# Kernel optimization log

Hardware: AMD Instinct MI355X
Metric: run time of the kernel (lower is better)

Reference implementation:

```python
import jax, jax.numpy as jnp
import numpy as np

D = 256; H = 4; HD = 64; WBAND = 64; KLOC = 8; EMAK = 256
SUMDECAY = 0.9; STATEDECAY = 0.9; STEP = 0.5


def _dwconv(x, kern, pad):
    # x: (B,T,D), kern: (D,1,K) cross-correlation taps, causal left pad
    lhs = jnp.transpose(x, (0, 2, 1))
    out = jax.lax.conv_general_dilated(
        lhs, kern, (1,), [(pad, 0)],
        dimension_numbers=('NCH', 'OIH', 'NCH'),
        feature_group_count=x.shape[-1])
    return jnp.transpose(out, (0, 2, 1))


def _ln(x, g, b):
    m = jnp.mean(x, -1, keepdims=True)
    v = jnp.var(x, -1, keepdims=True)
    return (x - m) * jax.lax.rsqrt(v + 1e-5) * g + b


def _lin(x, w, b):
    return jnp.dot(x, w.T) + b


def _forward(parallel_repr, sequential_state, trajectory_summary, conv_w, conv_b,
             qkv_w, qkv_b, mo_w, mo_b, fg_w, fg_b, gkv_w, gkv_b, go_w, go_b,
             comb_w, comb_b, ffn1_w, ffn1_b, ffn2_w, ffn2_b, tr1_w, tr1_b,
             tr2_w, tr2_b, p2s_w, p2s_b, s2p_w, s2p_b,
             ln1_g, ln1_b, ln2_g, ln2_b, ln3_g, ln3_b, ln4_g, ln4_b):
    B, T, _ = parallel_repr.shape
    # Tier 1: local depthwise causal conv (window 8); torch pads both sides then slices [:T] == causal left pad
    local_history = _dwconv(parallel_repr, conv_w, KLOC - 1) + conv_b
    # Tier 2: banded causal attention (keep j in [i-63, i])
    qkv = _lin(parallel_repr, qkv_w, qkv_b).reshape(B, T, 3, H, HD)
    qkv = jnp.transpose(qkv, (2, 0, 3, 1, 4))  # (3,B,H,T,HD)
    q, k, v = qkv[0], qkv[1], qkv[2]
    idx = jnp.arange(T)
    band = (idx[:, None] >= idx[None, :]) & (idx[None, :] > idx[:, None] - WBAND)
    scores = jnp.einsum('bhqd,bhkd->bhqk', q, k) / jnp.sqrt(jnp.float32(HD))
    attn = jax.nn.softmax(jnp.where(band, scores, -1e9), -1)
    med = jnp.einsum('bhqk,bhkd->bhqd', attn, v)
    med = jnp.transpose(med, (0, 2, 1, 3)).reshape(B, T, D)
    med = _lin(med, mo_w, mo_b)
    fg = jax.nn.sigmoid(_lin(jnp.concatenate([parallel_repr, med], -1), fg_w, fg_b))
    medium_out = med * fg
    # Tier 3: causal cumulative (linear-attention style) global concepts
    gkv = _lin(parallel_repr, gkv_w, gkv_b)
    gk, gv = jnp.split(gkv, 2, -1)
    gk = jax.nn.elu(gk) + 1.0
    concepts = jnp.cumsum(gk * gv, 1) / (jnp.cumsum(gk, 1) + 1e-5)
    global_out = _lin(concepts, go_w, go_b)
    combined = _lin(jnp.concatenate([local_history, medium_out, global_out], -1), comb_w, comb_b)
    pr = _ln(parallel_repr + combined, ln1_g, ln1_b)
    # EMA summary via 256-tap causal depthwise conv: w[i] = (1-d)*d^i
    kE = min(T, EMAK)
    taps = (1.0 - SUMDECAY) * SUMDECAY ** jnp.arange(kE, dtype=jnp.float32)
    kern = jnp.broadcast_to(taps[::-1][None, None, :], (D, 1, kE))
    global_summary = _dwconv(pr, kern, kE - 1)
    guidance = _lin(pr, p2s_w, p2s_b)
    cs = jnp.concatenate([pr + 0.3 * guidance, global_summary], -1)
    deltas = jnp.tanh(_lin(jax.nn.gelu(_lin(cs, tr1_w, tr1_b), approximate=False), tr2_w, tr2_b))
    scaled = deltas * STEP
    # state accumulation via conv trick: acc[t] = sum_i d^i * delta[t-i]
    staps = STATEDECAY ** jnp.arange(kE, dtype=jnp.float32)
    skern = jnp.broadcast_to(staps[::-1][None, None, :], (D, 1, kE))
    acc = _dwconv(scaled, skern, kE - 1)
    dpow = STATEDECAY ** jnp.arange(1, T + 1, dtype=jnp.float32)
    pre_ln = sequential_state[:, None, :] * dpow[None, :, None] + acc
    states = _ln(pre_ln, ln3_g, ln3_b)
    seq_g = _lin(states, s2p_w, s2p_b)
    ffn = _lin(jax.nn.gelu(_lin(pr + 0.3 * seq_g, ffn1_w, ffn1_b), approximate=False), ffn2_w, ffn2_b)
    pr_out = _ln(pr + ffn, ln2_g, ln2_b)
    final_state = _ln(states[:, -1, :], ln4_g, ln4_b)
    final_traj = global_summary[:, -1, :]
    return pr_out, final_state, final_traj


def setup_inputs():
    key = jax.random.key(0)
    ks = jax.random.split(key, 20)
    B, T = 4, 2048
    s = 0.02
    def w(i, shape):
        return jax.random.normal(ks[i], shape, jnp.float32) * s
    return {
        'parallel_repr': jax.random.normal(ks[0], (B, T, D), jnp.float32),
        'sequential_state': jax.random.normal(ks[1], (B, D), jnp.float32),
        'trajectory_summary': jax.random.normal(ks[2], (B, D), jnp.float32),
        'conv_w': w(3, (D, 1, KLOC)), 'conv_b': jnp.zeros((D,)),
        'qkv_w': w(4, (3 * D, D)), 'qkv_b': jnp.zeros((3 * D,)),
        'mo_w': w(5, (D, D)), 'mo_b': jnp.zeros((D,)),
        'fg_w': w(6, (D, 2 * D)), 'fg_b': jnp.zeros((D,)),
        'gkv_w': w(7, (2 * D, D)), 'gkv_b': jnp.zeros((2 * D,)),
        'go_w': w(8, (D, D)), 'go_b': jnp.zeros((D,)),
        'comb_w': w(9, (D, 3 * D)), 'comb_b': jnp.zeros((D,)),
        'ffn1_w': w(10, (4 * D, D)), 'ffn1_b': jnp.zeros((4 * D,)),
        'ffn2_w': w(11, (D, 4 * D)), 'ffn2_b': jnp.zeros((D,)),
        'tr1_w': w(12, (2 * D, 2 * D)), 'tr1_b': jnp.zeros((2 * D,)),
        'tr2_w': w(13, (D, 2 * D)), 'tr2_b': jnp.zeros((D,)),
        'p2s_w': w(14, (D, D)), 'p2s_b': jnp.zeros((D,)),
        's2p_w': w(15, (D, D)), 's2p_b': jnp.zeros((D,)),
        'ln1_g': jnp.ones((D,)), 'ln1_b': jnp.zeros((D,)),
        'ln2_g': jnp.ones((D,)), 'ln2_b': jnp.zeros((D,)),
        'ln3_g': jnp.ones((D,)), 'ln3_b': jnp.zeros((D,)),
        'ln4_g': jnp.ones((D,)), 'ln4_b': jnp.zeros((D,)),
    }


def reference(parallel_repr, sequential_state, trajectory_summary, conv_w, conv_b,
              qkv_w, qkv_b, mo_w, mo_b, fg_w, fg_b, gkv_w, gkv_b, go_w, go_b,
              comb_w, comb_b, ffn1_w, ffn1_b, ffn2_w, ffn2_b, tr1_w, tr1_b,
              tr2_w, tr2_b, p2s_w, p2s_b, s2p_w, s2p_b,
              ln1_g, ln1_b, ln2_g, ln2_b, ln3_g, ln3_b, ln4_g, ln4_b):
    return _forward(parallel_repr, sequential_state, trajectory_summary, conv_w, conv_b,
                    qkv_w, qkv_b, mo_w, mo_b, fg_w, fg_b, gkv_w, gkv_b, go_w, go_b,
                    comb_w, comb_b, ffn1_w, ffn1_b, ffn2_w, ffn2_b, tr1_w, tr1_b,
                    tr2_w, tr2_b, p2s_w, p2s_b, s2p_w, s2p_b,
                    ln1_g, ln1_b, ln2_g, ln2_b, ln3_g, ln3_b, ln4_g, ln4_b)
```

## Files before the change

kernel.cpp:

```cpp
#include <hip/hip_runtime.h>
#include <hip/hip_bf16.h>
#include <math.h>

#define D_  256
#define T_  2048
#define B_  4
#define M_  (B_*T_)
#define H_  4
#define HD_ 64

#define NC_ 64
#define LCH (T_/NC_)

enum { OP_NONE=0, OP_SIGMUL=1, OP_ADDAUX=2, OP_AXPBY=3, OP_GELU=4, OP_TANHHALF=5 };

typedef unsigned short u16;
typedef short short8 __attribute__((ext_vector_type(8)));
typedef float f32x4  __attribute__((ext_vector_type(4)));

__device__ __forceinline__ float gelu_f(float x){ return 0.5f*x*(1.0f+erff(x*0.70710678118654752f)); }
__device__ __forceinline__ float sigmoid_f(float x){ return 1.0f/(1.0f+expf(-x)); }

__device__ __forceinline__ unsigned pk2(float a, float b){
    __hip_bfloat162 h = __float22bfloat162_rn(make_float2(a,b));
    union { __hip_bfloat162 h; unsigned u; } c; c.h = h; return c.u;
}
__device__ __forceinline__ float bfu(u16 u){ return __uint_as_float(((unsigned)u)<<16); }
__device__ __forceinline__ u16 bf1(float x){ return (u16)(pk2(x,x)&0xffffu); }

#define OFF_QKV   0u
#define OFF_MO    327680u
#define OFF_FG    393216u
#define OFF_GO    524288u
#define OFF_COMB  589824u
#define OFF_FFN1  786432u
#define OFF_FFN2  1048576u
#define OFF_TR1   1310720u
#define OFF_TR2   1572864u
#define OFF_P2S   1703936u
#define OFF_S2P   1769472u
#define NWELEM    1835008u
#define NXELEM    2097152u

__global__ __launch_bounds__(256) void cvt_k(
    const float* __restrict__ qkv_w, const float* __restrict__ gkv_w,
    const float* __restrict__ qkv_b, const float* __restrict__ gkv_b,
    const float* __restrict__ mo_w,  const float* __restrict__ fg_w,
    const float* __restrict__ go_w,  const float* __restrict__ comb_w,
    const float* __restrict__ ffn1_w,const float* __restrict__ ffn2_w,
    const float* __restrict__ tr1_w, const float* __restrict__ tr2_w,
    const float* __restrict__ p2s_w, const float* __restrict__ s2p_w,
    const float* __restrict__ X,
    u16* __restrict__ Wh, u16* __restrict__ Xh, float* __restrict__ bq)
{
    size_t i = ((size_t)blockIdx.x*256 + threadIdx.x)*4;
    if (i < NWELEM){
        const float* s; size_t base;
        if      (i < OFF_MO)  { s=(i<196608)?qkv_w:gkv_w; base=(i<196608)?0:196608; }
        else if (i < OFF_FG)  { s=mo_w;   base=OFF_MO; }
        else if (i < OFF_GO)  { s=fg_w;   base=OFF_FG; }
        else if (i < OFF_COMB){ s=go_w;   base=OFF_GO; }
        else if (i < OFF_FFN1){ s=comb_w; base=OFF_COMB; }
        else if (i < OFF_FFN2){ s=ffn1_w; base=OFF_FFN1; }
        else if (i < OFF_TR1) { s=ffn2_w; base=OFF_FFN2; }
        else if (i < OFF_TR2) { s=tr1_w;  base=OFF_TR1; }
        else if (i < OFF_P2S) { s=tr2_w;  base=OFF_TR2; }
        else if (i < OFF_S2P) { s=p2s_w;  base=OFF_P2S; }
        else                  { s=s2p_w;  base=OFF_S2P; }
        float4 v = *(const float4*)(s + (i-base));
        *(uint2*)(Wh + i) = (uint2){ pk2(v.x,v.y), pk2(v.z,v.w) };
    } else if (i < NWELEM + NXELEM){
        size_t j = i - NWELEM;
        float4 v = *(const float4*)(X + j);
        *(uint2*)(Xh + j) = (uint2){ pk2(v.x,v.y), pk2(v.z,v.w) };
    } else if (i < NWELEM + NXELEM + 1280){
        size_t j = i - (NWELEM + NXELEM);
        #pragma unroll
        for (int k=0;k<4;++k){
            size_t e = j + k;
            bq[e] = (e < 768) ? qkv_b[e] : gkv_b[e-768];
        }
    }
}

__global__ __launch_bounds__(256) void gemm_k(
    const u16* __restrict__ A0, const u16* __restrict__ W0, int ldw0, int K0,
    const u16* __restrict__ A1, const u16* __restrict__ W1, int ldw1, int K1,
    const u16* __restrict__ A2, const u16* __restrict__ W2, int ldw2, int K2,
    const float* __restrict__ bias, const void* __restrict__ aux, int aux_bf16,
    void* __restrict__ C, int ldc, int c_bf16, int op, int ncol, u16* __restrict__ vt)
{
    __shared__ u16 As[64*64];
    __shared__ u16 Ws[64*64];

    const int q8   = gridDim.x >> 3;
    const int lid  = (blockIdx.x & 7)*q8 + (blockIdx.x >> 3);
    const int brow = lid / ncol;
    const int bcol = lid - brow*ncol;
    const int row0 = brow*64, col0 = bcol*64;

    const int tid  = threadIdx.x;
    const int lane = tid & 63, wid = tid >> 6;
    const int wm = (wid >> 1)*32, wn = (wid & 1)*32;
    const int l15 = lane & 15, l4 = lane >> 4;
    const int srow = tid >> 3;
    const int sc8  = (tid & 7) * 8;

    f32x4 acc[2][2];
    #pragma unroll
    for (int i=0;i<2;++i)
        #pragma unroll
        for (int j=0;j<2;++j) acc[i][j] = (f32x4){0.f,0.f,0.f,0.f};

    uint4 ra0, ra1, rw0, rw1;

    auto loadtile = [&](const u16* A, const u16* W, int ldw, int K, int kb){
        const u16* ga = A + (size_t)(row0+srow)*K + kb + sc8;
        ra0 = *(const uint4*)ga;
        ra1 = *(const uint4*)(ga + (size_t)32*K);
        const u16* gw = W + (size_t)(col0+srow)*ldw + kb + sc8;
        rw0 = *(const uint4*)gw;
        rw1 = *(const uint4*)(gw + (size_t)32*ldw);
    };
    auto storetile = [&](){
        const int i0 = (srow*64 + sc8) ^ ((srow&7)<<3);
        *(uint4*)&As[i0] = ra0;  *(uint4*)&Ws[i0] = rw0;
        const int r2 = srow + 32;
        const int i1 = (r2*64 + sc8) ^ ((r2&7)<<3);
        *(uint4*)&As[i1] = ra1;  *(uint4*)&Ws[i1] = rw1;
    };
    auto mfma_tile = [&](){
        #pragma unroll
        for (int ks=0;ks<2;++ks){
            const int koff = ks*32 + l4*8;
            short8 af[2], bf[2];
            #pragma unroll
            for (int f=0;f<2;++f){
                const int ar = wm + f*16 + l15;
                af[f] = *(const short8*)&As[(ar*64 + koff) ^ ((ar&7)<<3)];
                const int brn = wn + f*16 + l15;
                bf[f] = *(const short8*)&Ws[(brn*64 + koff) ^ ((brn&7)<<3)];
            }
            #pragma unroll
            for (int fm=0;fm<2;++fm)
                #pragma unroll
                for (int fn=0;fn<2;++fn)
                    acc[fm][fn] = __builtin_amdgcn_mfma_f32_16x16x32_bf16(
                        af[fm], bf[fn], acc[fm][fn], 0, 0, 0);
        }
    };

    const u16* Ac = A0; const u16* Wc = W0; int ldwc = ldw0, Kc = K0, kb = 0;
    loadtile(Ac, Wc, ldwc, Kc, 0);
    while (true){
        __syncthreads();
        storetile();
        __syncthreads();
        int nkb = kb + 64;
        const u16* nA = Ac; const u16* nW = Wc; int nld = ldwc, nK = Kc;
        bool have_next = true;
        if (nkb >= Kc){
            if (Ac == A0 && A1){ nA = A1; nW = W1; nld = ldw1; nK = K1; nkb = 0; }
            else if (Ac == A1 && A2){ nA = A2; nW = W2; nld = ldw2; nK = K2; nkb = 0; }
            else have_next = false;
        }
        if (have_next) loadtile(nA, nW, nld, nK, nkb);
        mfma_tile();
        if (!have_next) break;
        Ac = nA; Wc = nW; ldwc = nld; Kc = nK; kb = nkb;
    }

    #pragma unroll
    for (int fn=0;fn<2;++fn){
        const int n = col0 + wn + fn*16 + l15;
        const float bv = bias[n];
        const bool vwr = (vt != nullptr) && (n >= 512) && (n < 768);
        #pragma unroll
        for (int fm=0;fm<2;++fm){
            #pragma unroll
            for (int j=0;j<4;++j){
                const int m = row0 + wm + fm*16 + l4*4 + j;
                float v = acc[fm][fn][j] + bv;
                if (op==OP_GELU)          v = gelu_f(v);
                else if (op==OP_TANHHALF) v = 0.5f*tanhf(v);
                else if (op!=OP_NONE){
                    const size_t ai = (size_t)m*D_ + n;
                    const float a = aux_bf16 ? bfu(((const u16*)aux)[ai])
                                             : ((const float*)aux)[ai];
                    if (op==OP_SIGMUL)      v = a*sigmoid_f(v);
                    else if (op==OP_ADDAUX) v = v + a;
                    else                    v = a + 0.3f*v;
                }
                if (c_bf16) ((u16*)C)[(size_t)m*ldc + n] = bf1(v);
                else        ((float*)C)[(size_t)m*ldc + n] = v;
                if (vwr){
                    const int hh = (n-512)>>6, dd = (n-512)&63;
                    const int bb = m >> 11, tt = m & (T_-1);
                    vt[(((size_t)(bb*H_ + hh))*64 + dd)*T_ + tt] = bf1(v);
                }
            }
        }
    }
}

__global__ __launch_bounds__(256) void conv_k(const float* __restrict__ X,
    const float* __restrict__ w, const float* __restrict__ bias, u16* __restrict__ out)
{
    int idx = blockIdx.x*256 + threadIdx.x;
    int d = idx & (D_-1);
    int bt = idx >> 8;
    int t = bt & (T_-1);
    float acc = bias[d];
    const float* xp = X + (size_t)bt*D_ + d;
    const float* wp = w + d*8;
    #pragma unroll
    for (int j=0;j<8;++j){
        int tt = t - 7 + j;
        if (tt >= 0) acc += xp[(size_t)(j-7)*D_] * wp[j];
    }
    out[idx] = bf1(acc);
}

__global__ __launch_bounds__(256) void attn_k(const u16* __restrict__ QKVG,
    const u16* __restrict__ VT, u16* __restrict__ MED)
{
    __shared__ u16 Kl[128*64];
    __shared__ u16 Ql[64*64];
    __shared__ u16 Vl[64*128];
    const int b = blockIdx.z, h = blockIdx.y;
    const int t0 = blockIdx.x * 64;
    const int kb0 = t0 - 64;
    const int tid = threadIdx.x;

    {
        const int r0 = tid >> 3, c8 = (tid & 7) * 8;
        #pragma unroll
        for (int rep=0;rep<4;++rep){
            const int r = r0 + rep*32;
            const int kg = kb0 + r;
            uint4 pk = {0,0,0,0};
            if (kg >= 0)
                pk = *(const uint4*)(QKVG + ((size_t)(b*T_ + kg))*1280 + 256 + h*HD_ + c8);
            *(uint4*)&Kl[(r*64 + c8) ^ ((r&7)<<3)] = pk;
        }
        #pragma unroll
        for (int rep=0;rep<2;++rep){
            const int r = r0 + rep*32;
            uint4 pq = *(const uint4*)(QKVG + ((size_t)(b*T_ + t0 + r))*1280 + h*HD_ + c8);
            *(uint4*)&Ql[(r*64 + c8) ^ ((r&7)<<3)] = pq;
        }
    }
    {
        const int d0 = tid >> 4, c8 = (tid & 15) * 8;
        #pragma unroll
        for (int rep=0;rep<4;++rep){
            const int d = d0 + rep*16;
            uint4 pv = {0,0,0,0};
            if (kb0 + c8 >= 0)
                pv = *(const uint4*)(VT + ((size_t)((b*H_ + h)*64 + d))*T_ + kb0 + c8);
            *(uint4*)&Vl[(d*128 + c8) ^ ((d&7)<<3)] = pv;
        }
    }
    __syncthreads();

    const int lane = tid & 63, w = tid >> 6;
    const int l15 = lane & 15, l4 = lane >> 4;

    short8 bq[2];
    {
        const int qr = w*16 + l15;
        bq[0] = *(const short8*)&Ql[(qr*64 +      l4*8) ^ ((qr&7)<<3)];
        bq[1] = *(const short8*)&Ql[(qr*64 + 32 + l4*8) ^ ((qr&7)<<3)];
    }

    f32x4 s[8];
    #pragma unroll
    for (int kf=0;kf<8;++kf){
        const int kr = kf*16 + l15;
        short8 a0 = *(const short8*)&Kl[(kr*64 +      l4*8) ^ ((kr&7)<<3)];
        short8 a1 = *(const short8*)&Kl[(kr*64 + 32 + l4*8) ^ ((kr&7)<<3)];
        f32x4 acc = (f32x4){0.f,0.f,0.f,0.f};
        acc = __builtin_amdgcn_mfma_f32_16x16x32_bf16(a0, bq[0], acc, 0,0,0);
        acc = __builtin_amdgcn_mfma_f32_16x16x32_bf16(a1, bq[1], acc, 0,0,0);
        s[kf] = acc;
    }

    const int qg = t0 + w*16 + l15;
    float m = -1e30f;
    #pragma unroll
    for (int kf=0;kf<8;++kf){
        #pragma unroll
        for (int j=0;j<4;++j){
            const int kg = kb0 + kf*16 + l4*4 + j;
            const int diff = qg - kg;
            const float v = (kg >= 0 && diff >= 0 && diff < 64) ? s[kf][j]*0.125f : -1e30f;
            s[kf][j] = v;
            m = fmaxf(m, v);
        }
    }
    m = fmaxf(m, __shfl_xor(m,16));
    m = fmaxf(m, __shfl_xor(m,32));
    float lsum = 0.f;
    unsigned lo[8], hi[8];
    #pragma unroll
    for (int kf=0;kf<8;++kf){
        const float p0 = expf(s[kf][0]-m), p1 = expf(s[kf][1]-m);
        const float p2 = expf(s[kf][2]-m), p3 = expf(s[kf][3]-m);
        lsum += (p0+p1)+(p2+p3);
        lo[kf] = pk2(p0,p1);
        hi[kf] = pk2(p2,p3);
    }
    lsum += __shfl_xor(lsum,16);
    lsum += __shfl_xor(lsum,32);
    const float inv = 1.f/lsum;

    f32x4 o[4];
    #pragma unroll
    for (int df=0;df<4;++df) o[df] = (f32x4){0.f,0.f,0.f,0.f};
    const int baseLane = l15 + ((l4&1)<<5);
    const bool hiHalf = (l4>>1) != 0;
    #pragma unroll
    for (int kb=0;kb<4;++kb){
        const int x0 = __shfl((int)lo[2*kb],   baseLane);
        const int x1 = __shfl((int)hi[2*kb],   baseLane);
        const int x2 = __shfl((int)lo[2*kb],   baseLane+16);
        const int x3 = __shfl((int)hi[2*kb],   baseLane+16);
        const int y0 = __shfl((int)lo[2*kb+1], baseLane);
        const int y1 = __shfl((int)hi[2*kb+1], baseLane);
        const int y2 = __shfl((int)lo[2*kb+1], baseLane+16);
        const int y3 = __shfl((int)hi[2*kb+1], baseLane+16);
        int4 afi;
        afi.x = hiHalf ? y0 : x0;
        afi.y = hiHalf ? y1 : x1;
        afi.z = hiHalf ? y2 : x2;
        afi.w = hiHalf ? y3 : x3;
        union { int4 i; short8 s; } cv; cv.i = afi;
        #pragma unroll
        for (int df=0;df<4;++df){
            const int vr = df*16 + l15;
            short8 bv = *(const short8*)&Vl[(vr*128 + kb*32 + l4*8) ^ ((vr&7)<<3)];
            o[df] = __builtin_amdgcn_mfma_f32_16x16x32_bf16(cv.s, bv, o[df], 0,0,0);
        }
    }

    #pragma unroll
    for (int j=0;j<4;++j){
        const float invj = __shfl(inv, l4*4 + j);
        const int mrow = b*T_ + t0 + w*16 + l4*4 + j;
        u16* op = MED + (size_t)mrow*D_ + h*HD_ + l15;
        #pragma unroll
        for (int df=0;df<4;++df)
            op[df*16] = bf1(o[df][j] * invj);
    }
}

__global__ __launch_bounds__(256) void scan1_p1(const u16* __restrict__ QKVG,
    float* __restrict__ CA, float* __restrict__ CC)
{
    const int d = threadIdx.x, c = blockIdx.x, b = blockIdx.y;
    const u16* base = QKVG + ((size_t)(b*T_ + c*LCH))*1280;
    float sgk=0.f, sgkv=0.f;
    for (int t=0;t<LCH;++t){
        float gk = bfu(base[(size_t)t*1280 + 768 + d]);
        gk = gk > 0.f ? gk + 1.f : expf(gk);
        float gv = bfu(base[(size_t)t*1280 + 1024 + d]);
        sgk += gk; sgkv += gk*gv;
    }
    CA[((size_t)b*NC_ + c)*D_ + d] = sgk;
    CC[((size_t)b*NC_ + c)*D_ + d] = sgkv;
}

__global__ void scan1_p2(float* __restrict__ CA, float* __restrict__ CC)
{
    int idx = blockIdx.x*256 + threadIdx.x;
    int d = idx & (D_-1), b = idx >> 8;
    float sa=0.f, sc=0.f;
    for (int c=0;c<NC_;++c){
        size_t o = ((size_t)b*NC_ + c)*D_ + d;
        float a = CA[o], cc = CC[o];
        CA[o] = sa; CC[o] = sc;
        sa += a; sc += cc;
    }
}

__global__ __launch_bounds__(256) void scan1_p3(const u16* __restrict__ QKVG,
    const float* __restrict__ CA, const float* __restrict__ CC, u16* __restrict__ CONC)
{
    const int d = threadIdx.x, c = blockIdx.x, b = blockIdx.y;
    float sgk  = CA[((size_t)b*NC_ + c)*D_ + d];
    float sgkv = CC[((size_t)b*NC_ + c)*D_ + d];
    const u16* base = QKVG + ((size_t)(b*T_ + c*LCH))*1280;
    u16* out = CONC + ((size_t)(b*T_ + c*LCH))*D_ + d;
    for (int t=0;t<LCH;++t){
        float gk = bfu(base[(size_t)t*1280 + 768 + d]);
        gk = gk > 0.f ? gk + 1.f : expf(gk);
        float gv = bfu(base[(size_t)t*1280 + 1024 + d]);
        sgk += gk; sgkv += gk*gv;
        out[(size_t)t*D_] = bf1(sgkv / (sgk + 1e-5f));
    }
}

__global__ __launch_bounds__(256) void ema_p1(const float* __restrict__ X,
    float* __restrict__ CARRY, float alpha)
{
    const int d = threadIdx.x, c = blockIdx.x, b = blockIdx.y;
    const float* xp = X + ((size_t)(b*T_ + c*LCH))*D_ + d;
    float g = 0.f;
    for (int t=0;t<LCH;++t) g = 0.9f*g + alpha*xp[(size_t)t*D_];
    CARRY[((size_t)b*NC_ + c)*D_ + d] = g;
}

__global__ void ema_p2(float* __restrict__ CARRY, float* __restrict__ traj)
{
    int idx = blockIdx.x*256 + threadIdx.x;
    int d = idx & (D_-1), b = idx >> 8;
    const float dL = powf(0.9f, (float)LCH);
    float run = 0.f;
    for (int c=0;c<NC_;++c){
        size_t o = ((size_t)b*NC_ + c)*D_ + d;
        float loc = CARRY[o];
        CARRY[o] = run;
        run = loc + dL*run;
    }
    if (traj) traj[b*D_ + d] = run;
}

__global__ __launch_bounds__(256) void ema_p3h(const float* __restrict__ X,
    const float* __restrict__ CARRY, u16* __restrict__ OUT, float alpha)
{
    const int d = threadIdx.x, c = blockIdx.x, b = blockIdx.y;
    float g = CARRY[((size_t)b*NC_ + c)*D_ + d];
    const float* xp = X + ((size_t)(b*T_ + c*LCH))*D_ + d;
    u16* op = OUT + ((size_t)(b*T_ + c*LCH))*D_ + d;
    for (int t=0;t<LCH;++t){
        g = 0.9f*g + alpha*xp[(size_t)t*D_];
        op[(size_t)t*D_] = bf1(g);
    }
}

__global__ __launch_bounds__(256) void ema_p3_state(const float* __restrict__ X,
    const float* __restrict__ CARRY, const float* __restrict__ SEQ, float* __restrict__ OUT)
{
    const int d = threadIdx.x, c = blockIdx.x, b = blockIdx.y;
    float a = CARRY[((size_t)b*NC_ + c)*D_ + d];
    const float ss = SEQ[b*D_ + d];
    float dp = powf(0.9f, (float)(c*LCH + 1));
    const float* xp = X + ((size_t)(b*T_ + c*LCH))*D_ + d;
    float* op = OUT + ((size_t)(b*T_ + c*LCH))*D_ + d;
    for (int t=0;t<LCH;++t){
        a = 0.9f*a + xp[(size_t)t*D_];
        op[(size_t)t*D_] = fmaf(ss, dp, a);
        dp *= 0.9f;
    }
}

__global__ __launch_bounds__(256) void ln_k(const float* __restrict__ in,
    const float* __restrict__ g, const float* __restrict__ b,
    float* __restrict__ out, u16* __restrict__ out2)
{
    int row  = blockIdx.x*4 + (threadIdx.x>>6);
    int lane = threadIdx.x & 63;
    const float* ip = in + (size_t)row*D_ + lane*4;
    float4 x = *(const float4*)ip;
    float s  = x.x+x.y+x.z+x.w;
    float s2 = x.x*x.x + x.y*x.y + x.z*x.z + x.w*x.w;
    #pragma unroll
    for (int o=1;o<64;o<<=1){ s += __shfl_xor(s,o); s2 += __shfl_xor(s2,o); }
    float mean = s * (1.f/256.f);
    float var  = s2 * (1.f/256.f) - mean*mean;
    float rs = rsqrtf(var + 1e-5f);
    int db = lane*4;
    float4 r;
    r.x=(x.x-mean)*rs*g[db+0]+b[db+0];
    r.y=(x.y-mean)*rs*g[db+1]+b[db+1];
    r.z=(x.z-mean)*rs*g[db+2]+b[db+2];
    r.w=(x.w-mean)*rs*g[db+3]+b[db+3];
    *(float4*)(out + (size_t)row*D_ + db) = r;
    if (out2)
        *(uint2*)(out2 + (size_t)row*D_ + db) = (uint2){ pk2(r.x,r.y), pk2(r.z,r.w) };
}

__global__ __launch_bounds__(256) void ln3_k(const float* __restrict__ in,
    const float* __restrict__ g3, const float* __restrict__ b3, u16* __restrict__ states,
    const float* __restrict__ g4, const float* __restrict__ b4, float* __restrict__ fsout)
{
    int row  = blockIdx.x*4 + (threadIdx.x>>6);
    int lane = threadIdx.x & 63;
    const float* ip = in + (size_t)row*D_ + lane*4;
    float4 x = *(const float4*)ip;
    float s  = x.x+x.y+x.z+x.w;
    float s2 = x.x*x.x + x.y*x.y + x.z*x.z + x.w*x.w;
    #pragma unroll
    for (int o=1;o<64;o<<=1){ s += __shfl_xor(s,o); s2 += __shfl_xor(s2,o); }
    float mean = s * (1.f/256.f);
    float var  = s2 * (1.f/256.f) - mean*mean;
    float rs = rsqrtf(var + 1e-5f);
    int db = lane*4;
    float4 st;
    st.x=(x.x-mean)*rs*g3[db+0]+b3[db+0];
    st.y=(x.y-mean)*rs*g3[db+1]+b3[db+1];
    st.z=(x.z-mean)*rs*g3[db+2]+b3[db+2];
    st.w=(x.w-mean)*rs*g3[db+3]+b3[db+3];
    *(uint2*)(states + (size_t)row*D_ + db) = (uint2){ pk2(st.x,st.y), pk2(st.z,st.w) };

    if ((row & (T_-1)) == T_-1){
        float u  = st.x+st.y+st.z+st.w;
        float u2 = st.x*st.x + st.y*st.y + st.z*st.z + st.w*st.w;
        #pragma unroll
        for (int o=1;o<64;o<<=1){ u += __shfl_xor(u,o); u2 += __shfl_xor(u2,o); }
        float m2 = u * (1.f/256.f);
        float v2 = u2 * (1.f/256.f) - m2*m2;
        float r2 = rsqrtf(v2 + 1e-5f);
        float4 fs;
        fs.x=(st.x-m2)*r2*g4[db+0]+b4[db+0];
        fs.y=(st.y-m2)*r2*g4[db+1]+b4[db+1];
        fs.z=(st.z-m2)*r2*g4[db+2]+b4[db+2];
        fs.w=(st.w-m2)*r2*g4[db+3]+b4[db+3];
        *(float4*)(fsout + (size_t)(row>>11)*D_ + db) = fs;
    }
}

extern "C" void kernel_launch(void* const* d_in, const int* in_sizes, int n_in,
                              void* d_out, int out_size, void* d_ws, size_t ws_size,
                              hipStream_t stream)
{
    const float* X     = (const float*)d_in[0];
    const float* SEQ   = (const float*)d_in[1];
    const float* conv_w= (const float*)d_in[3];
    const float* conv_b= (const float*)d_in[4];
    const float* qkv_w = (const float*)d_in[5];
    const float* qkv_b = (const float*)d_in[6];
    const float* mo_w  = (const float*)d_in[7];
    const float* mo_b  = (const float*)d_in[8];
    const float* fg_w  = (const float*)d_in[9];
    const float* fg_b  = (const float*)d_in[10];
    const float* gkv_w = (const float*)d_in[11];
    const float* gkv_b = (const float*)d_in[12];
    const float* go_w  = (const float*)d_in[13];
    const float* go_b  = (const float*)d_in[14];
    const float* comb_w= (const float*)d_in[15];
    const float* comb_b= (const float*)d_in[16];
    const float* ffn1_w= (const float*)d_in[17];
    const float* ffn1_b= (const float*)d_in[18];
    const float* ffn2_w= (const float*)d_in[19];
    const float* ffn2_b= (const float*)d_in[20];
    const float* tr1_w = (const float*)d_in[21];
    const float* tr1_b = (const float*)d_in[22];
    const float* tr2_w = (const float*)d_in[23];
    const float* tr2_b = (const float*)d_in[24];
    const float* p2s_w = (const float*)d_in[25];
    const float* p2s_b = (const float*)d_in[26];
    const float* s2p_w = (const float*)d_in[27];
    const float* s2p_b = (const float*)d_in[28];
    const float* ln1_g = (const float*)d_in[29];
    const float* ln1_b = (const float*)d_in[30];
    const float* ln2_g = (const float*)d_in[31];
    const float* ln2_b = (const float*)d_in[32];
    const float* ln3_g = (const float*)d_in[33];
    const float* ln3_b = (const float*)d_in[34];
    const float* ln4_g = (const float*)d_in[35];
    const float* ln4_b = (const float*)d_in[36];

    char* p = (char*)d_ws;
    auto alloc = [&](size_t bytes)->char*{ char* r = p; p += (bytes + 255) & ~(size_t)255; return r; };

    u16*   QKVG = (u16*)  alloc((size_t)M_*1280*2);
    u16*   Wh   = (u16*)  alloc((size_t)NWELEM*2);
    float* bq   = (float*)alloc(1280*4);
    u16*   Xh   = (u16*)  alloc((size_t)M_*256*2);
    u16*   VTh  = (u16*)  alloc((size_t)M_*256*2);
    u16*   MED  = (u16*)  alloc((size_t)M_*256*2);
    u16*   MED2 = (u16*)  alloc((size_t)M_*256*2);
    u16*   LH   = (u16*)  alloc((size_t)M_*256*2);
    u16*   CONC = (u16*)  alloc((size_t)M_*256*2);
    u16*   GOUT = (u16*)  alloc((size_t)M_*256*2);
    u16*   MOUT = (u16*)  alloc((size_t)M_*256*2);
    float* PRE1 = (float*)alloc((size_t)M_*256*4);
    float* PR   = (float*)alloc((size_t)M_*256*4);
    u16*   PRh  = (u16*)  alloc((size_t)M_*256*2);
    u16*   GSUM = (u16*)  alloc((size_t)M_*256*2);
    u16*   CS1  = (u16*)  alloc((size_t)M_*256*2);
    u16*   H1   = (u16*)  alloc((size_t)M_*512*2);
    float* SCALED=(float*)alloc((size_t)M_*256*4);
    float* PRE3 = (float*)alloc((size_t)M_*256*4);
    u16*   STATESh=(u16*) alloc((size_t)M_*256*2);
    u16*   FFNIN= (u16*)  alloc((size_t)M_*256*2);
    u16*   H2   = (u16*)  alloc((size_t)M_*1024*2);
    float* PRE2 = (float*)alloc((size_t)M_*256*4);
    float* CAR0 = (float*)alloc((size_t)B_*NC_*D_*4);
    float* CAR1 = (float*)alloc((size_t)B_*NC_*D_*4);

    float* out_pr = (float*)d_out;
    float* out_fs = out_pr + (size_t)M_*256;
    float* out_tj = out_fs + B_*256;

    const dim3 blk256(256);
    const dim3 scan_grid(NC_, B_);
    const int NR = M_/64;

    cvt_k<<<dim3(3842), blk256, 0, stream>>>(
        qkv_w, gkv_w, qkv_b, gkv_b, mo_w, fg_w, go_w, comb_w,
        ffn1_w, ffn2_w, tr1_w, tr2_w, p2s_w, s2p_w, X, Wh, Xh, bq);
    gemm_k<<<dim3(NR*20), blk256, 0, stream>>>(
        Xh, Wh+OFF_QKV, 256, 256,  nullptr,nullptr,0,0,  nullptr,nullptr,0,0,
        bq, nullptr, 0, QKVG, 1280, 1, OP_NONE, 20, VTh);
    conv_k<<<dim3(M_*D_/256), blk256, 0, stream>>>(X, conv_w, conv_b, LH);
    attn_k<<<dim3(T_/64, H_, B_), blk256, 0, stream>>>(QKVG, VTh, MED);
    gemm_k<<<dim3(NR*4), blk256, 0, stream>>>(
        MED, Wh+OFF_MO, 256, 256,  nullptr,nullptr,0,0,  nullptr,nullptr,0,0,
        mo_b, nullptr, 0, MED2, 256, 1, OP_NONE, 4, nullptr);
    scan1_p1<<<scan_grid, blk256, 0, stream>>>(QKVG, CAR0, CAR1);
    scan1_p2<<<dim3(4), blk256, 0, stream>>>(CAR0, CAR1);
    scan1_p3<<<scan_grid, blk256, 0, stream>>>(QKVG, CAR0, CAR1, CONC);
    gemm_k<<<dim3(NR*4), blk256, 0, stream>>>(
        CONC, Wh+OFF_GO, 256, 256,  nullptr,nullptr,0,0,  nullptr,nullptr,0,0,
        go_b, nullptr, 0, GOUT, 256, 1, OP_NONE, 4, nullptr);
    gemm_k<<<dim3(NR*4), blk256, 0, stream>>>(
        Xh, Wh+OFF_FG, 512, 256,  MED2, Wh+OFF_FG+256, 512, 256,  nullptr,nullptr,0,0,
        fg_b, MED2, 1, MOUT, 256, 1, OP_SIGMUL, 4, nullptr);
    gemm_k<<<dim3(NR*4), blk256, 0, stream>>>(
        LH, Wh+OFF_COMB, 768, 256,  MOUT, Wh+OFF_COMB+256, 768, 256,  GOUT, Wh+OFF_COMB+512, 768, 256,
        comb_b, X, 0, PRE1, 256, 0, OP_ADDAUX, 4, nullptr);
    ln_k<<<dim3(M_/4), blk256, 0, stream>>>(PRE1, ln1_g, ln1_b, PR, PRh);
    ema_p1<<<scan_grid, blk256, 0, stream>>>(PR, CAR0, 0.1f);
    ema_p2<<<dim3(4), blk256, 0, stream>>>(CAR0, out_tj);
    ema_p3h<<<scan_grid, blk256, 0, stream>>>(PR, CAR0, GSUM, 0.1f);
    gemm_k<<<dim3(NR*4), blk256, 0, stream>>>(
        PRh, Wh+OFF_P2S, 256, 256,  nullptr,nullptr,0,0,  nullptr,nullptr,0,0,
        p2s_b, PR, 0, CS1, 256, 1, OP_AXPBY, 4, nullptr);
    gemm_k<<<dim3(NR*8), blk256, 0, stream>>>(
        CS1, Wh+OFF_TR1, 512, 256,  GSUM, Wh+OFF_TR1+256, 512, 256,  nullptr,nullptr,0,0,
        tr1_b, nullptr, 0, H1, 512, 1, OP_GELU, 8, nullptr);
    gemm_k<<<dim3(NR*4), blk256, 0, stream>>>(
        H1, Wh+OFF_TR2, 512, 512,  nullptr,nullptr,0,0,  nullptr,nullptr,0,0,
        tr2_b, nullptr, 0, SCALED, 256, 0, OP_TANHHALF, 4, nullptr);
    ema_p1<<<scan_grid, blk256, 0, stream>>>(SCALED, CAR0, 1.0f);
    ema_p2<<<dim3(4), blk256, 0, stream>>>(CAR0, nullptr);
    ema_p3_state<<<scan_grid, blk256, 0, stream>>>(SCALED, CAR0, SEQ, PRE3);
    ln3_k<<<dim3(M_/4), blk256, 0, stream>>>(PRE3, ln3_g, ln3_b, STATESh, ln4_g, ln4_b, out_fs);
    gemm_k<<<dim3(NR*4), blk256, 0, stream>>>(
        STATESh, Wh+OFF_S2P, 256, 256,  nullptr,nullptr,0,0,  nullptr,nullptr,0,0,
        s2p_b, PR, 0, FFNIN, 256, 1, OP_AXPBY, 4, nullptr);
    gemm_k<<<dim3(NR*16), blk256, 0, stream>>>(
        FFNIN, Wh+OFF_FFN1, 256, 256,  nullptr,nullptr,0,0,  nullptr,nullptr,0,0,
        ffn1_b, nullptr, 0, H2, 1024, 1, OP_GELU, 16, nullptr);
    gemm_k<<<dim3(NR*4), blk256, 0, stream>>>(
        H2, Wh+OFF_FFN2, 1024, 1024,  nullptr,nullptr,0,0,  nullptr,nullptr,0,0,
        ffn2_b, PR, 0, PRE2, 256, 0, OP_ADDAUX, 4, nullptr);
    ln_k<<<dim3(M_/4), blk256, 0, stream>>>(PRE2, ln2_g, ln2_b, out_pr, nullptr);
}
```

Measured before the change: 255.8 us.

## Widen GEMM K-tile, drop V-transpose buffer and fold scan carry passes

The GEMM now stages 128-wide K tiles (twice the LDS, half the sync iterations) with a 16-row XOR swizzle. The transposed V buffer written in the QKV GEMM epilogue is removed, and attention transposes V into LDS itself from QKVG. The separate carry-propagation kernels (scan1_p2, ema_p2) are removed, with each chunk block summing prior chunk carries serially. The conv and EMA kernels read bf16 inputs instead of fp32. Fewer launches and less scattered global writes are traded for redundant per-block carry loops, scalar LDS transpose stores and slightly lower input precision.

```diff
diff --git a/kernel.cpp b/kernel.cpp
--- a/kernel.cpp
+++ b/kernel.cpp
@@ -88,10 +88,10 @@
     const u16* __restrict__ A1, const u16* __restrict__ W1, int ldw1, int K1,
     const u16* __restrict__ A2, const u16* __restrict__ W2, int ldw2, int K2,
     const float* __restrict__ bias, const void* __restrict__ aux, int aux_bf16,
-    void* __restrict__ C, int ldc, int c_bf16, int op, int ncol, u16* __restrict__ vt)
-{
-    __shared__ u16 As[64*64];
-    __shared__ u16 Ws[64*64];
+    void* __restrict__ C, int ldc, int c_bf16, int op, int ncol)
+{
+    __shared__ u16 As[64*128];
+    __shared__ u16 Ws[64*128];
 
     const int q8   = gridDim.x >> 3;
     const int lid  = (blockIdx.x & 7)*q8 + (blockIdx.x >> 3);
@@ -103,8 +103,8 @@
     const int lane = tid & 63, wid = tid >> 6;
     const int wm = (wid >> 1)*32, wn = (wid & 1)*32;
     const int l15 = lane & 15, l4 = lane >> 4;
-    const int srow = tid >> 3;
-    const int sc8  = (tid & 7) * 8;
+    const int srow = tid >> 2;
+    const int sc   = (tid & 3) * 32;
 
     f32x4 acc[2][2];
     #pragma unroll
@@ -112,34 +112,33 @@
         #pragma unroll
         for (int j=0;j<2;++j) acc[i][j] = (f32x4){0.f,0.f,0.f,0.f};
 
-    uint4 ra0, ra1, rw0, rw1;
+    uint4 ra[4], rw[4];
 
     auto loadtile = [&](const u16* A, const u16* W, int ldw, int K, int kb){
-        const u16* ga = A + (size_t)(row0+srow)*K + kb + sc8;
-        ra0 = *(const uint4*)ga;
-        ra1 = *(const uint4*)(ga + (size_t)32*K);
-        const u16* gw = W + (size_t)(col0+srow)*ldw + kb + sc8;
-        rw0 = *(const uint4*)gw;
-        rw1 = *(const uint4*)(gw + (size_t)32*ldw);
+        const u16* ga = A + (size_t)(row0+srow)*K + kb + sc;
+        const u16* gw = W + (size_t)(col0+srow)*ldw + kb + sc;
+        #pragma unroll
+        for (int c=0;c<4;++c){ ra[c] = *(const uint4*)(ga + c*8); rw[c] = *(const uint4*)(gw + c*8); }
     };
     auto storetile = [&](){
-        const int i0 = (srow*64 + sc8) ^ ((srow&7)<<3);
-        *(uint4*)&As[i0] = ra0;  *(uint4*)&Ws[i0] = rw0;
-        const int r2 = srow + 32;
-        const int i1 = (r2*64 + sc8) ^ ((r2&7)<<3);
-        *(uint4*)&As[i1] = ra1;  *(uint4*)&Ws[i1] = rw1;
+        #pragma unroll
+        for (int c=0;c<4;++c){
+            const int idx = (srow*128 + sc + c*8) ^ ((srow&15)<<3);
+            *(uint4*)&As[idx] = ra[c];
+            *(uint4*)&Ws[idx] = rw[c];
+        }
     };
     auto mfma_tile = [&](){
         #pragma unroll
-        for (int ks=0;ks<2;++ks){
+        for (int ks=0;ks<4;++ks){
             const int koff = ks*32 + l4*8;
             short8 af[2], bf[2];
             #pragma unroll
             for (int f=0;f<2;++f){
                 const int ar = wm + f*16 + l15;
-                af[f] = *(const short8*)&As[(ar*64 + koff) ^ ((ar&7)<<3)];
+                af[f] = *(const short8*)&As[(ar*128 + koff) ^ ((ar&15)<<3)];
                 const int brn = wn + f*16 + l15;
-                bf[f] = *(const short8*)&Ws[(brn*64 + koff) ^ ((brn&7)<<3)];
+                bf[f] = *(const short8*)&Ws[(brn*128 + koff) ^ ((brn&15)<<3)];
             }
             #pragma unroll
             for (int fm=0;fm<2;++fm)
@@ -156,7 +155,7 @@
         __syncthreads();
         storetile();
         __syncthreads();
-        int nkb = kb + 64;
+        int nkb = kb + 128;
         const u16* nA = Ac; const u16* nW = Wc; int nld = ldwc, nK = Kc;
         bool have_next = true;
         if (nkb >= Kc){
@@ -174,7 +173,6 @@
     for (int fn=0;fn<2;++fn){
         const int n = col0 + wn + fn*16 + l15;
         const float bv = bias[n];
-        const bool vwr = (vt != nullptr) && (n >= 512) && (n < 768);
         #pragma unroll
         for (int fm=0;fm<2;++fm){
             #pragma unroll
@@ -193,17 +191,12 @@
                 }
                 if (c_bf16) ((u16*)C)[(size_t)m*ldc + n] = bf1(v);
                 else        ((float*)C)[(size_t)m*ldc + n] = v;
-                if (vwr){
-                    const int hh = (n-512)>>6, dd = (n-512)&63;
-                    const int bb = m >> 11, tt = m & (T_-1);
-                    vt[(((size_t)(bb*H_ + hh))*64 + dd)*T_ + tt] = bf1(v);
-                }
             }
         }
     }
 }
 
-__global__ __launch_bounds__(256) void conv_k(const float* __restrict__ X,
+__global__ __launch_bounds__(256) void conv_k(const u16* __restrict__ Xh,
     const float* __restrict__ w, const float* __restrict__ bias, u16* __restrict__ out)
 {
     int idx = blockIdx.x*256 + threadIdx.x;
@@ -211,18 +204,18 @@
     int bt = idx >> 8;
     int t = bt & (T_-1);
     float acc = bias[d];
-    const float* xp = X + (size_t)bt*D_ + d;
+    const u16* xp = Xh + (size_t)bt*D_ + d;
     const float* wp = w + d*8;
     #pragma unroll
     for (int j=0;j<8;++j){
         int tt = t - 7 + j;
-        if (tt >= 0) acc += xp[(size_t)(j-7)*D_] * wp[j];
+        if (tt >= 0) acc += bfu(xp[(size_t)(j-7)*D_]) * wp[j];
     }
     out[idx] = bf1(acc);
 }
 
 __global__ __launch_bounds__(256) void attn_k(const u16* __restrict__ QKVG,
-    const u16* __restrict__ VT, u16* __restrict__ MED)
+    u16* __restrict__ MED)
 {
     __shared__ u16 Kl[128*64];
     __shared__ u16 Ql[64*64];
@@ -238,27 +231,25 @@
         for (int rep=0;rep<4;++rep){
             const int r = r0 + rep*32;
             const int kg = kb0 + r;
-            uint4 pk = {0,0,0,0};
-            if (kg >= 0)
-                pk = *(const uint4*)(QKVG + ((size_t)(b*T_ + kg))*1280 + 256 + h*HD_ + c8);
+            uint4 pk = {0,0,0,0}, pv = {0,0,0,0};
+            if (kg >= 0){
+                const u16* gp = QKVG + ((size_t)(b*T_ + kg))*1280 + h*HD_ + c8;
+                pk = *(const uint4*)(gp + 256);
+                pv = *(const uint4*)(gp + 512);
+            }
             *(uint4*)&Kl[(r*64 + c8) ^ ((r&7)<<3)] = pk;
+            const u16* pvu = (const u16*)&pv;
+            #pragma unroll
+            for (int j=0;j<8;++j){
+                const int d = c8 + j;
+                Vl[(d*128 + r) ^ ((d&15)<<3)] = pvu[j];
+            }
         }
         #pragma unroll
         for (int rep=0;rep<2;++rep){
             const int r = r0 + rep*32;
             uint4 pq = *(const uint4*)(QKVG + ((size_t)(b*T_ + t0 + r))*1280 + h*HD_ + c8);
             *(uint4*)&Ql[(r*64 + c8) ^ ((r&7)<<3)] = pq;
-        }
-    }
-    {
-        const int d0 = tid >> 4, c8 = (tid & 15) * 8;
-        #pragma unroll
-        for (int rep=0;rep<4;++rep){
-            const int d = d0 + rep*16;
-            uint4 pv = {0,0,0,0};
-            if (kb0 + c8 >= 0)
-                pv = *(const uint4*)(VT + ((size_t)((b*H_ + h)*64 + d))*T_ + kb0 + c8);
-            *(uint4*)&Vl[(d*128 + c8) ^ ((d&7)<<3)] = pv;
         }
     }
     __syncthreads();
@@ -338,7 +329,7 @@
         #pragma unroll
         for (int df=0;df<4;++df){
             const int vr = df*16 + l15;
-            short8 bv = *(const short8*)&Vl[(vr*128 + kb*32 + l4*8) ^ ((vr&7)<<3)];
+            short8 bv = *(const short8*)&Vl[(vr*128 + kb*32 + l4*8) ^ ((vr&15)<<3)];
             o[df] = __builtin_amdgcn_mfma_f32_16x16x32_bf16(cv.s, bv, o[df], 0,0,0);
         }
     }
@@ -370,25 +361,15 @@
     CC[((size_t)b*NC_ + c)*D_ + d] = sgkv;
 }
 
-__global__ void scan1_p2(float* __restrict__ CA, float* __restrict__ CC)
-{
-    int idx = blockIdx.x*256 + threadIdx.x;
-    int d = idx & (D_-1), b = idx >> 8;
-    float sa=0.f, sc=0.f;
-    for (int c=0;c<NC_;++c){
-        size_t o = ((size_t)b*NC_ + c)*D_ + d;
-        float a = CA[o], cc = CC[o];
-        CA[o] = sa; CC[o] = sc;
-        sa += a; sc += cc;
-    }
-}
-
 __global__ __launch_bounds__(256) void scan1_p3(const u16* __restrict__ QKVG,
     const float* __restrict__ CA, const float* __restrict__ CC, u16* __restrict__ CONC)
 {
     const int d = threadIdx.x, c = blockIdx.x, b = blockIdx.y;
-    float sgk  = CA[((size_t)b*NC_ + c)*D_ + d];
-    float sgkv = CC[((size_t)b*NC_ + c)*D_ + d];
+    float sgk = 0.f, sgkv = 0.f;
+    for (int cc=0; cc<c; ++cc){
+        sgk  += CA[((size_t)b*NC_ + cc)*D_ + d];
+        sgkv += CC[((size_t)b*NC_ + cc)*D_ + d];
+    }
     const u16* base = QKVG + ((size_t)(b*T_ + c*LCH))*1280;
     u16* out = CONC + ((size_t)(b*T_ + c*LCH))*D_ + d;
     for (int t=0;t<LCH;++t){
@@ -400,6 +381,16 @@
     }
 }
 
+__global__ __launch_bounds__(256) void ema_p1h(const u16* __restrict__ X,
+    float* __restrict__ CARRY, float alpha)
+{
+    const int d = threadIdx.x, c = blockIdx.x, b = blockIdx.y;
+    const u16* xp = X + ((size_t)(b*T_ + c*LCH))*D_ + d;
+    float g = 0.f;
+    for (int t=0;t<LCH;++t) g = 0.9f*g + alpha*bfu(xp[(size_t)t*D_]);
+    CARRY[((size_t)b*NC_ + c)*D_ + d] = g;
+}
+
 __global__ __launch_bounds__(256) void ema_p1(const float* __restrict__ X,
     float* __restrict__ CARRY, float alpha)
 {
@@ -410,39 +401,30 @@
     CARRY[((size_t)b*NC_ + c)*D_ + d] = g;
 }
 
-__global__ void ema_p2(float* __restrict__ CARRY, float* __restrict__ traj)
-{
-    int idx = blockIdx.x*256 + threadIdx.x;
-    int d = idx & (D_-1), b = idx >> 8;
+__global__ __launch_bounds__(256) void ema_p3h(const u16* __restrict__ X,
+    const float* __restrict__ CARRY, u16* __restrict__ OUT, float alpha,
+    float* __restrict__ traj)
+{
+    const int d = threadIdx.x, c = blockIdx.x, b = blockIdx.y;
     const float dL = powf(0.9f, (float)LCH);
-    float run = 0.f;
-    for (int c=0;c<NC_;++c){
-        size_t o = ((size_t)b*NC_ + c)*D_ + d;
-        float loc = CARRY[o];
-        CARRY[o] = run;
-        run = loc + dL*run;
-    }
-    if (traj) traj[b*D_ + d] = run;
-}
-
-__global__ __launch_bounds__(256) void ema_p3h(const float* __restrict__ X,
-    const float* __restrict__ CARRY, u16* __restrict__ OUT, float alpha)
-{
-    const int d = threadIdx.x, c = blockIdx.x, b = blockIdx.y;
-    float g = CARRY[((size_t)b*NC_ + c)*D_ + d];
-    const float* xp = X + ((size_t)(b*T_ + c*LCH))*D_ + d;
+    float g = 0.f;
+    for (int cc=0; cc<c; ++cc) g = CARRY[((size_t)b*NC_ + cc)*D_ + d] + dL*g;
+    const u16* xp = X + ((size_t)(b*T_ + c*LCH))*D_ + d;
     u16* op = OUT + ((size_t)(b*T_ + c*LCH))*D_ + d;
     for (int t=0;t<LCH;++t){
-        g = 0.9f*g + alpha*xp[(size_t)t*D_];
+        g = 0.9f*g + alpha*bfu(xp[(size_t)t*D_]);
         op[(size_t)t*D_] = bf1(g);
     }
+    if (c == NC_-1) traj[b*D_ + d] = g;
 }
 
 __global__ __launch_bounds__(256) void ema_p3_state(const float* __restrict__ X,
     const float* __restrict__ CARRY, const float* __restrict__ SEQ, float* __restrict__ OUT)
 {
     const int d = threadIdx.x, c = blockIdx.x, b = blockIdx.y;
-    float a = CARRY[((size_t)b*NC_ + c)*D_ + d];
+    const float dL = powf(0.9f, (float)LCH);
+    float a = 0.f;
+    for (int cc=0; cc<c; ++cc) a = CARRY[((size_t)b*NC_ + cc)*D_ + d] + dL*a;
     const float ss = SEQ[b*D_ + d];
     float dp = powf(0.9f, (float)(c*LCH + 1));
     const float* xp = X + ((size_t)(b*T_ + c*LCH))*D_ + d;
@@ -568,7 +550,6 @@
     u16*   Wh   = (u16*)  alloc((size_t)NWELEM*2);
     float* bq   = (float*)alloc(1280*4);
     u16*   Xh   = (u16*)  alloc((size_t)M_*256*2);
-    u16*   VTh  = (u16*)  alloc((size_t)M_*256*2);
     u16*   MED  = (u16*)  alloc((size_t)M_*256*2);
     u16*   MED2 = (u16*)  alloc((size_t)M_*256*2);
     u16*   LH   = (u16*)  alloc((size_t)M_*256*2);
@@ -603,49 +584,46 @@
         ffn1_w, ffn2_w, tr1_w, tr2_w, p2s_w, s2p_w, X, Wh, Xh, bq);
     gemm_k<<<dim3(NR*20), blk256, 0, stream>>>(
         Xh, Wh+OFF_QKV, 256, 256,  nullptr,nullptr,0,0,  nullptr,nullptr,0,0,
-        bq, nullptr, 0, QKVG, 1280, 1, OP_NONE, 20, VTh);
-    conv_k<<<dim3(M_*D_/256), blk256, 0, stream>>>(X, conv_w, conv_b, LH);
-    attn_k<<<dim3(T_/64, H_, B_), blk256, 0, stream>>>(QKVG, VTh, MED);
+        bq, nullptr, 0, QKVG, 1280, 1, OP_NONE, 20);
+    conv_k<<<dim3(M_*D_/256), blk256, 0, stream>>>(Xh, conv_w, conv_b, LH);
+    attn_k<<<dim3(T_/64, H_, B_), blk256, 0, stream>>>(QKVG, MED);
     gemm_k<<<dim3(NR*4), blk256, 0, stream>>>(
         MED, Wh+OFF_MO, 256, 256,  nullptr,nullptr,0,0,  nullptr,nullptr,0,0,
-        mo_b, nullptr, 0, MED2, 256, 1, OP_NONE, 4, nullptr);
+        mo_b, nullptr, 0, MED2, 256, 1, OP_NONE, 4);
     scan1_p1<<<scan_grid, blk256, 0, stream>>>(QKVG, CAR0, CAR1);
-    scan1_p2<<<dim3(4), blk256, 0, stream>>>(CAR0, CAR1);
     scan1_p3<<<scan_grid, blk256, 0, stream>>>(QKVG, CAR0, CAR1, CONC);
     gemm_k<<<dim3(NR*4), blk256, 0, stream>>>(
         CONC, Wh+OFF_GO, 256, 256,  nullptr,nullptr,0,0,  nullptr,nullptr,0,0,
-        go_b, nullptr, 0, GOUT, 256, 1, OP_NONE, 4, nullptr);
+        go_b, nullptr, 0, GOUT, 256, 1, OP_NONE, 4);
     gemm_k<<<dim3(NR*4), blk256, 0, stream>>>(
         Xh, Wh+OFF_FG, 512, 256,  MED2, Wh+OFF_FG+256, 512, 256,  nullptr,nullptr,0,0,
-        fg_b, MED2, 1, MOUT, 256, 1, OP_SIGMUL, 4, nullptr);
+        fg_b, MED2, 1, MOUT, 256, 1, OP_SIGMUL, 4);
     gemm_k<<<dim3(NR*4), blk256, 0, stream>>>(
         LH, Wh+OFF_COMB, 768, 256,  MOUT, Wh+OFF_COMB+256, 768, 256,  GOUT, Wh+OFF_COMB+512, 768, 256,
-        comb_b, X, 0, PRE1, 256, 0, OP_ADDAUX, 4, nullptr);
+        comb_b, X, 0, PRE1, 256, 0, OP_ADDAUX, 4);
     ln_k<<<dim3(M_/4), blk256, 0, stream>>>(PRE1, ln1_g, ln1_b, PR, PRh);
-    ema_p1<<<scan_grid, blk256, 0, stream>>>(PR, CAR0, 0.1f);
-    ema_p2<<<dim3(4), blk256, 0, stream>>>(CAR0, out_tj);
-    ema_p3h<<<scan_grid, blk256, 0, stream>>>(PR, CAR0, GSUM, 0.1f);
+    ema_p1h<<<scan_grid, blk256, 0, stream>>>(PRh, CAR0, 0.1f);
+    ema_p3h<<<scan_grid, blk256, 0, stream>>>(PRh, CAR0, GSUM, 0.1f, out_tj);
     gemm_k<<<dim3(NR*4), blk256, 0, stream>>>(
         PRh, Wh+OFF_P2S, 256, 256,  nullptr,nullptr,0,0,  nullptr,nullptr,0,0,
-        p2s_b, PR, 0, CS1, 256, 1, OP_AXPBY, 4, nullptr);
+        p2s_b, PR, 0, CS1, 256, 1, OP_AXPBY, 4);
     gemm_k<<<dim3(NR*8), blk256, 0, stream>>>(
         CS1, Wh+OFF_TR1, 512, 256,  GSUM, Wh+OFF_TR1+256, 512, 256,  nullptr,nullptr,0,0,
-        tr1_b, nullptr, 0, H1, 512, 1, OP_GELU, 8, nullptr);
+        tr1_b, nullptr, 0, H1, 512, 1, OP_GELU, 8);
     gemm_k<<<dim3(NR*4), blk256, 0, stream>>>(
         H1, Wh+OFF_TR2, 512, 512,  nullptr,nullptr,0,0,  nullptr,nullptr,0,0,
-        tr2_b, nullptr, 0, SCALED, 256, 0, OP_TANHHALF, 4, nullptr);
+        tr2_b, nullptr, 0, SCALED, 256, 0, OP_TANHHALF, 4);
     ema_p1<<<scan_grid, blk256, 0, stream>>>(SCALED, CAR0, 1.0f);
-    ema_p2<<<dim3(4), blk256, 0, stream>>>(CAR0, nullptr);
     ema_p3_state<<<scan_grid, blk256, 0, stream>>>(SCALED, CAR0, SEQ, PRE3);
     ln3_k<<<dim3(M_/4), blk256, 0, stream>>>(PRE3, ln3_g, ln3_b, STATESh, ln4_g, ln4_b, out_fs);
     gemm_k<<<dim3(NR*4), blk256, 0, stream>>>(
         STATESh, Wh+OFF_S2P, 256, 256,  nullptr,nullptr,0,0,  nullptr,nullptr,0,0,
-        s2p_b, PR, 0, FFNIN, 256, 1, OP_AXPBY, 4, nullptr);
+        s2p_b, PR, 0, FFNIN, 256, 1, OP_AXPBY, 4);
     gemm_k<<<dim3(NR*16), blk256, 0, stream>>>(
         FFNIN, Wh+OFF_FFN1, 256, 256,  nullptr,nullptr,0,0,  nullptr,nullptr,0,0,
-        ffn1_b, nullptr, 0, H2, 1024, 1, OP_GELU, 16, nullptr);
+        ffn1_b, nullptr, 0, H2, 1024, 1, OP_GELU, 16);
     gemm_k<<<dim3(NR*4), blk256, 0, stream>>>(
         H2, Wh+OFF_FFN2, 1024, 1024,  nullptr,nullptr,0,0,  nullptr,nullptr,0,0,
-        ffn2_b, PR, 0, PRE2, 256, 0, OP_ADDAUX, 4, nullptr);
+        ffn2_b, PR, 0, PRE2, 256, 0, OP_ADDAUX, 4);
     ln_k<<<dim3(M_/4), blk256, 0, stream>>>(PRE2, ln2_g, ln2_b, out_pr, nullptr);
 }
```

New measurement: 488.8 us. 91.1% more time.
